# Kernel tuning notes

Measured on AMD Instinct MI355X. Metric: run time of the kernel, lower is better.

Reference implementation:

```python
import jax, jax.numpy as jnp
import numpy as np

B_SZ, T, I, H = 32, 2048, 128, 256

def setup_inputs() -> dict:
    key = jax.random.key(0)
    k1, k2, k3, k4 = jax.random.split(key, 4)
    x = jax.random.normal(k1, (B_SZ, T, I), dtype=jnp.float32)
    A = jax.random.normal(k2, (H, H), dtype=jnp.float32) * 0.01
    Bm = jax.random.normal(k3, (I, H), dtype=jnp.float32) * 0.01
    C = jax.random.normal(k4, (H, H), dtype=jnp.float32) * 0.01
    return {"x": x, "A": A, "Bm": Bm, "C": C}

def reference(x, A, Bm, C):
    # Precompute input projection for all timesteps: [B, T, H]
    xB = jnp.einsum('bti,ih->bth', x, Bm)
    h0 = jnp.zeros((x.shape[0], A.shape[0]), dtype=x.dtype)

    def step(h, xb_t):
        h = jnp.tanh(h @ A + xb_t)  # [B, H]
        return h, h

    # scan over time: xB transposed to [T, B, H]
    _, hs = jax.lax.scan(step, h0, jnp.swapaxes(xB, 0, 1))
    # outputs: h_t @ C at every step -> [B, T, H]
    out = jnp.einsum('tbh,hk->btk', hs, C)
    return out
```

## Files before the change

### kernel.cpp

```cpp
#include <hip/hip_runtime.h>
#include <math.h>

#define B_SZ 32
#define T_LEN 2048
#define I_DIM 128
#define H_DIM 256
#define ROWS 32

__global__ __launch_bounds__(256) void xb_proj(const float* __restrict__ x,
                                               const float* __restrict__ Bm,
                                               float* __restrict__ xB) {
    __shared__ float4 xt[ROWS][I_DIM / 4 + 1];
    const int tid = threadIdx.x;
    const int j = tid;
    const long r0 = (long)blockIdx.x * ROWS;

    const float4* xg = (const float4*)(x + r0 * I_DIM);
#pragma unroll
    for (int i = 0; i < 4; ++i) {
        int f = tid + i * 256;
        int rr = f >> 5;
        int kg = f & 31;
        xt[rr][kg] = xg[rr * 32 + kg];
    }
    __syncthreads();

    float acc[ROWS];
#pragma unroll
    for (int r = 0; r < ROWS; ++r) acc[r] = 0.f;

    for (int k = 0; k < I_DIM; k += 4) {
        float w0 = Bm[(k + 0) * H_DIM + j];
        float w1 = Bm[(k + 1) * H_DIM + j];
        float w2 = Bm[(k + 2) * H_DIM + j];
        float w3 = Bm[(k + 3) * H_DIM + j];
#pragma unroll
        for (int r = 0; r < ROWS; ++r) {
            float4 hv = xt[r][k >> 2];
            acc[r] = fmaf(hv.x, w0, acc[r]);
            acc[r] = fmaf(hv.y, w1, acc[r]);
            acc[r] = fmaf(hv.z, w2, acc[r]);
            acc[r] = fmaf(hv.w, w3, acc[r]);
        }
    }
#pragma unroll
    for (int r = 0; r < ROWS; ++r)
        xB[(r0 + r) * H_DIM + j] = acc[r];
}

__global__ __launch_bounds__(512, 2) void rnn_scan(const float* __restrict__ A,
                                                   const float* __restrict__ xB,
                                                   float* __restrict__ hs) {
    __shared__ __align__(16) float h[H_DIM];
    __shared__ float red[H_DIM];
    const int tid = threadIdx.x;
    const int j = tid & 255;
    const int kh = tid >> 8;
    const int b = blockIdx.x;

    float Areg[128];
#pragma unroll
    for (int kk = 0; kk < 128; ++kk)
        Areg[kk] = A[(kh * 128 + kk) * H_DIM + j];

    if (tid < H_DIM) h[tid] = 0.f;

    const float* xbp = xB + (long)b * T_LEN * H_DIM + j;
    float* hp = hs + (long)b * T_LEN * H_DIM + j;
    float xb_next = xbp[0];

    __syncthreads();

    for (int t = 0; t < T_LEN; ++t) {
        float p0 = 0.f, p1 = 0.f, p2 = 0.f, p3 = 0.f;
        const float4* h4 = (const float4*)&h[kh * 128];
#pragma unroll
        for (int kk = 0; kk < 128; kk += 4) {
            float4 hv = h4[kk >> 2];
            p0 = fmaf(hv.x, Areg[kk + 0], p0);
            p1 = fmaf(hv.y, Areg[kk + 1], p1);
            p2 = fmaf(hv.z, Areg[kk + 2], p2);
            p3 = fmaf(hv.w, Areg[kk + 3], p3);
        }
        float partial = (p0 + p1) + (p2 + p3);
        if (kh == 0) red[j] = partial;
        __syncthreads();
        if (kh == 1) {
            float y = partial + red[j] + xb_next;
            float hn = tanhf(y);
            h[j] = hn;
            hp[(long)t * H_DIM] = hn;
            if (t + 1 < T_LEN) xb_next = xbp[(long)(t + 1) * H_DIM];
        }
        __syncthreads();
    }
}

__global__ __launch_bounds__(256) void out_proj(float* __restrict__ hs_out,
                                                const float* __restrict__ C) {
    __shared__ float4 ht[ROWS][H_DIM / 4 + 1];
    const int tid = threadIdx.x;
    const int j = tid;
    const long r0 = (long)blockIdx.x * ROWS;

    const float4* hg = (const float4*)(hs_out + r0 * H_DIM);
#pragma unroll
    for (int i = 0; i < 8; ++i) {
        int f = tid + i * 256;
        int rr = f >> 6;
        int kg = f & 63;
        ht[rr][kg] = hg[rr * 64 + kg];
    }
    __syncthreads();

    float acc[ROWS];
#pragma unroll
    for (int r = 0; r < ROWS; ++r) acc[r] = 0.f;

    for (int k = 0; k < H_DIM; k += 4) {
        float w0 = C[(k + 0) * H_DIM + j];
        float w1 = C[(k + 1) * H_DIM + j];
        float w2 = C[(k + 2) * H_DIM + j];
        float w3 = C[(k + 3) * H_DIM + j];
#pragma unroll
        for (int r = 0; r < ROWS; ++r) {
            float4 hv = ht[r][k >> 2];
            acc[r] = fmaf(hv.x, w0, acc[r]);
            acc[r] = fmaf(hv.y, w1, acc[r]);
            acc[r] = fmaf(hv.z, w2, acc[r]);
            acc[r] = fmaf(hv.w, w3, acc[r]);
        }
    }
#pragma unroll
    for (int r = 0; r < ROWS; ++r)
        hs_out[(r0 + r) * H_DIM + j] = acc[r];
}

extern "C" void kernel_launch(void* const* d_in, const int* in_sizes, int n_in,
                              void* d_out, int out_size, void* d_ws, size_t ws_size,
                              hipStream_t stream) {
    const float* x  = (const float*)d_in[0];
    const float* A  = (const float*)d_in[1];
    const float* Bm = (const float*)d_in[2];
    const float* C  = (const float*)d_in[3];
    float* out = (float*)d_out;
    float* xB  = (float*)d_ws;

    const int R = B_SZ * T_LEN;

    xb_proj<<<R / ROWS, 256, 0, stream>>>(x, Bm, xB);
    rnn_scan<<<B_SZ, 512, 0, stream>>>(A, xB, out);
    out_proj<<<R / ROWS, 256, 0, stream>>>(out, C);
}
```

Measured before the change: 1.969 ms.

## Restructure RNN scan with 1024 threads, shuffle reduction and double-buffered state

Rewrites the recurrent step so each group of 8 lanes splits the K dimension and reduces with warp shuffles rather than through shared memory. The hidden state is double-buffered, which removes one of the two block barriers per timestep. It also uses a fast exp-based tanh. The goal is to cut per-step latency on the serial critical path, at the cost of more threads per block and slightly lower tanh accuracy.

```diff
diff --git a/kernel.cpp b/kernel.cpp
--- a/kernel.cpp
+++ b/kernel.cpp
@@ -48,49 +48,71 @@
         xB[(r0 + r) * H_DIM + j] = acc[r];
 }
 
-__global__ __launch_bounds__(512, 2) void rnn_scan(const float* __restrict__ A,
-                                                   const float* __restrict__ xB,
-                                                   float* __restrict__ hs) {
-    __shared__ __align__(16) float h[H_DIM];
-    __shared__ float red[H_DIM];
+#define HS_STRIDE 36
+
+__global__ __launch_bounds__(1024) void rnn_scan(const float* __restrict__ A,
+                                                 const float* __restrict__ xB,
+                                                 float* __restrict__ hs) {
+    __shared__ __align__(16) float h[2][8 * HS_STRIDE];
     const int tid = threadIdx.x;
-    const int j = tid & 255;
-    const int kh = tid >> 8;
+    const int s = tid & 7;
+    const int p = tid >> 3;
     const int b = blockIdx.x;
 
-    float Areg[128];
+    float a0[32], a1[32];
 #pragma unroll
-    for (int kk = 0; kk < 128; ++kk)
-        Areg[kk] = A[(kh * 128 + kk) * H_DIM + j];
+    for (int kk = 0; kk < 32; ++kk) {
+        a0[kk] = A[(s * 32 + kk) * H_DIM + p];
+        a1[kk] = A[(s * 32 + kk) * H_DIM + p + 128];
+    }
 
-    if (tid < H_DIM) h[tid] = 0.f;
+    if (tid < 2 * 8 * HS_STRIDE) ((float*)h)[tid] = 0.f;
 
-    const float* xbp = xB + (long)b * T_LEN * H_DIM + j;
-    float* hp = hs + (long)b * T_LEN * H_DIM + j;
-    float xb_next = xbp[0];
+    const long base = (long)b * T_LEN * H_DIM;
+    const int jw = (s == 1) ? (p + 128) : p;
+    const float* xbp = xB + base + jw;
+    float* hp = hs + base + jw;
+    float xbn = (s < 2) ? xbp[0] : 0.f;
 
     __syncthreads();
 
     for (int t = 0; t < T_LEN; ++t) {
-        float p0 = 0.f, p1 = 0.f, p2 = 0.f, p3 = 0.f;
-        const float4* h4 = (const float4*)&h[kh * 128];
+        const float4* h4 = (const float4*)(&h[t & 1][0] + s * HS_STRIDE);
+        float y0a = 0.f, y0b = 0.f, y1a = 0.f, y1b = 0.f;
 #pragma unroll
-        for (int kk = 0; kk < 128; kk += 4) {
-            float4 hv = h4[kk >> 2];
-            p0 = fmaf(hv.x, Areg[kk + 0], p0);
-            p1 = fmaf(hv.y, Areg[kk + 1], p1);
-            p2 = fmaf(hv.z, Areg[kk + 2], p2);
-            p3 = fmaf(hv.w, Areg[kk + 3], p3);
+        for (int kk = 0; kk < 8; kk += 2) {
+            float4 hva = h4[kk];
+            float4 hvb = h4[kk + 1];
+            y0a = fmaf(hva.x, a0[kk * 4 + 0], y0a);
+            y0a = fmaf(hva.y, a0[kk * 4 + 1], y0a);
+            y0a = fmaf(hva.z, a0[kk * 4 + 2], y0a);
+            y0a = fmaf(hva.w, a0[kk * 4 + 3], y0a);
+            y1a = fmaf(hva.x, a1[kk * 4 + 0], y1a);
+            y1a = fmaf(hva.y, a1[kk * 4 + 1], y1a);
+            y1a = fmaf(hva.z, a1[kk * 4 + 2], y1a);
+            y1a = fmaf(hva.w, a1[kk * 4 + 3], y1a);
+            y0b = fmaf(hvb.x, a0[kk * 4 + 4], y0b);
+            y0b = fmaf(hvb.y, a0[kk * 4 + 5], y0b);
+            y0b = fmaf(hvb.z, a0[kk * 4 + 6], y0b);
+            y0b = fmaf(hvb.w, a0[kk * 4 + 7], y0b);
+            y1b = fmaf(hvb.x, a1[kk * 4 + 4], y1b);
+            y1b = fmaf(hvb.y, a1[kk * 4 + 5], y1b);
+            y1b = fmaf(hvb.z, a1[kk * 4 + 6], y1b);
+            y1b = fmaf(hvb.w, a1[kk * 4 + 7], y1b);
         }
-        float partial = (p0 + p1) + (p2 + p3);
-        if (kh == 0) red[j] = partial;
-        __syncthreads();
-        if (kh == 1) {
-            float y = partial + red[j] + xb_next;
-            float hn = tanhf(y);
-            h[j] = hn;
+        float y0 = y0a + y0b;
+        float y1 = y1a + y1b;
+        y0 += __shfl_xor(y0, 1); y1 += __shfl_xor(y1, 1);
+        y0 += __shfl_xor(y0, 2); y1 += __shfl_xor(y1, 2);
+        y0 += __shfl_xor(y0, 4); y1 += __shfl_xor(y1, 4);
+
+        if (s < 2) {
+            float y = ((s == 0) ? y0 : y1) + xbn;
+            float e = __expf(2.f * y);
+            float hn = 1.f - 2.f / (e + 1.f);
+            h[(t + 1) & 1][((jw >> 5) * HS_STRIDE) + (jw & 31)] = hn;
             hp[(long)t * H_DIM] = hn;
-            if (t + 1 < T_LEN) xb_next = xbp[(long)(t + 1) * H_DIM];
+            if (t + 1 < T_LEN) xbn = xbp[(long)(t + 1) * H_DIM];
         }
         __syncthreads();
     }
@@ -149,6 +171,6 @@
     const int R = B_SZ * T_LEN;
 
     xb_proj<<<R / ROWS, 256, 0, stream>>>(x, Bm, xB);
-    rnn_scan<<<B_SZ, 512, 0, stream>>>(A, xB, out);
+    rnn_scan<<<B_SZ, 1024, 0, stream>>>(A, xB, out);
     out_proj<<<R / ROWS, 256, 0, stream>>>(out, C);
 }
```

Result: faster. 1.857 ms (-5.7%).
